# Kernel optimization log

Hardware: AMD Instinct MI355X
Metric: run time of the kernel (lower is better)

## Reference

```python
import jax, jax.numpy as jnp
import numpy as np

B, C, H, W = 16, 256, 56, 56
PH, PW = 7, 7            # partition (window) size
HEADS, DH = 8, 32        # n_heads = C // head_dim
P = PH * PW              # tokens per window = 49
GH, GW = H // PH, W // PW
G = GH * GW              # number of windows = 64
MLP = 4                  # mlp_ratio
EPS = 1e-5
SCALE = C ** (-0.5)      # note: torch code scales by feat_dim, not head_dim


def _rel_index(h, w):
    coords = np.stack(np.meshgrid(np.arange(h), np.arange(w), indexing='ij'))  # [2,h,w]
    cf = coords.reshape(2, -1)
    rel = cf[:, :, None] - cf[:, None, :]              # [2,P,P]
    rel = rel.transpose(1, 2, 0)
    rel[:, :, 0] += h - 1
    rel[:, :, 1] += w - 1
    rel[:, :, 0] *= 2 * w - 1
    return rel.sum(-1).astype(np.int32)                # [P,P]


def setup_inputs() -> dict:
    key = jax.random.key(0)
    ks = jax.random.split(key, 8)
    std = 0.02
    return {
        'x': jax.random.normal(ks[0], (B, C, H, W), jnp.float32),
        'ln1_g': jnp.ones((C,), jnp.float32),
        'ln1_b': jnp.zeros((C,), jnp.float32),
        'wqkv': jax.random.normal(ks[1], (C, 3 * C), jnp.float32) * std,
        'bqkv': jnp.zeros((3 * C,), jnp.float32),
        'wmerge': jax.random.normal(ks[2], (C, C), jnp.float32) * std,
        'bmerge': jnp.zeros((C,), jnp.float32),
        'bias_table': jax.random.normal(ks[3], ((2 * PH - 1) * (2 * PW - 1), HEADS), jnp.float32) * std,
        'ln2_g': jnp.ones((C,), jnp.float32),
        'ln2_b': jnp.zeros((C,), jnp.float32),
        'w1': jax.random.normal(ks[4], (C, MLP * C), jnp.float32) * std,
        'b1': jnp.zeros((MLP * C,), jnp.float32),
        'w2': jax.random.normal(ks[5], (MLP * C, C), jnp.float32) * std,
        'b2': jnp.zeros((C,), jnp.float32),
        'rel_idx': jnp.asarray(_rel_index(PH, PW)),
    }


def _layernorm(x, g, b):
    mu = jnp.mean(x, axis=-1, keepdims=True)
    var = jnp.var(x, axis=-1, keepdims=True)
    return (x - mu) * jax.lax.rsqrt(var + EPS) * g + b


def reference(x, ln1_g, ln1_b, wqkv, bqkv, wmerge, bmerge, bias_table,
              ln2_g, ln2_b, w1, b1, w2, b2, rel_idx):
    # --- window partition: [B,C,H,W] -> [B,G,P,C]
    xw = x.reshape(B, C, GH, PH, GW, PW).transpose(0, 2, 4, 3, 5, 1).reshape(B, G, P, C)

    # --- relative-position attention block
    y = _layernorm(xw, ln1_g, ln1_b)
    qkv = y @ wqkv + bqkv                               # [B,G,P,3C]
    q, k, v = jnp.split(qkv, 3, axis=-1)
    q = q.reshape(B, G, P, HEADS, DH)
    k = k.reshape(B, G, P, HEADS, DH) * SCALE
    v = v.reshape(B, G, P, HEADS, DH)
    scores = jnp.einsum('bgihd,bgjhd->bghij', q, k)     # [B,G,H,P,P]
    bias = bias_table[rel_idx].transpose(2, 0, 1)       # [H,P,P]
    attn = jax.nn.softmax(scores + bias[None, None], axis=-1)
    out = jnp.einsum('bghij,bgjhd->bgihd', attn, v).reshape(B, G, P, C)
    out = out @ wmerge + bmerge
    xw = xw + out

    # --- MLP block
    z = _layernorm(xw, ln2_g, ln2_b)
    z = jax.nn.gelu(z @ w1 + b1, approximate=False) @ w2 + b2
    xw = xw + z

    # --- window departition: [B,G,P,C] -> [B,C,H,W]
    xo = xw.reshape(B, GH, GW, PH, PW, C).transpose(0, 5, 1, 3, 2, 4).reshape(B, C, H, W)
    return xo
```

## Files before the change

kernel.cpp:

```cpp
#include <hip/hip_runtime.h>
#include <hip/hip_bf16.h>

#define B_      16
#define C_      256
#define H_      56
#define W_      56
#define HW_     3136
#define G_      64
#define P_      49
#define NTOK    50176
#define HEADS_  8
#define DH_     32
#define SCALE_  0.0625f
#define EPS_    1e-5f

typedef short bf16x8 __attribute__((ext_vector_type(8)));
typedef short bf16x4_t __attribute__((ext_vector_type(4)));
typedef float f32x4  __attribute__((ext_vector_type(4)));
using bf16 = __hip_bfloat16;

__device__ __forceinline__ void gload16(const void* g, void* l) {
  __builtin_amdgcn_global_load_lds((const __attribute__((address_space(1))) void*)g,
                                   (__attribute__((address_space(3))) void*)l, 16, 0, 0);
}
__device__ __forceinline__ float b2f(short s) {
  union { float f; unsigned u; } v; v.u = ((unsigned)(unsigned short)s) << 16; return v.f;
}
__device__ __forceinline__ short f2b(float f) {
  union { float f; unsigned u; } v; v.f = f;
  unsigned r = (v.u + 0x7FFFu + ((v.u >> 16) & 1u)) >> 16;
  return (short)r;
}

__global__ __launch_bounds__(256)
void prep_kernel(const float* __restrict__ wqkv, const float* __restrict__ wmerge,
                 const float* __restrict__ w1, const float* __restrict__ w2,
                 const float* __restrict__ btab, const int* __restrict__ relidx,
                 bf16* __restrict__ wqkvT, bf16* __restrict__ wmergeT,
                 bf16* __restrict__ w1T, bf16* __restrict__ w2T,
                 short* __restrict__ bt)
{
  int idx = blockIdx.x * 256 + threadIdx.x;
  if (idx < 196608) { int n = idx >> 8, k = idx & 255;
    wqkvT[idx] = __float2bfloat16(wqkv[k * 768 + n]); return; }
  idx -= 196608;
  if (idx < 65536) { int n = idx >> 8, k = idx & 255;
    wmergeT[idx] = __float2bfloat16(wmerge[k * 256 + n]); return; }
  idx -= 65536;
  if (idx < 262144) { int n = idx >> 8, k = idx & 255;
    w1T[idx] = __float2bfloat16(w1[k * 1024 + n]); return; }
  idx -= 262144;
  if (idx < 262144) { int n = idx >> 10, k = idx & 1023;
    w2T[idx] = __float2bfloat16(w2[k * 256 + n]); return; }
  idx -= 262144;
  if (idx < 32768) {
    int h = idx >> 12, rest = idx & 4095;
    int key = rest >> 6, col = rest & 63;
    int q = col >> 2, qni = col & 3;
    int query = qni * 16 + q;
    float v = 0.f;
    if (key < P_ && query < P_) v = btab[relidx[query * P_ + key] * HEADS_ + h];
    bt[idx] = f2b(v);
  }
}

__global__ __launch_bounds__(256)
void ingest_kernel(const float* __restrict__ x, const float* __restrict__ gam,
                   const float* __restrict__ bet, short* __restrict__ xtok,
                   short* __restrict__ y)
{
  __shared__ short Lt[56 * 260];
  const int h = blockIdx.x % 56, b = blockIdx.x / 56;
  const int tid = threadIdx.x;

  const float* xb = x + (size_t)b * 256 * HW_ + h * 56;
#pragma unroll
  for (int i = 0; i < 14; i++) {
    int idx = i * 256 + tid;
    int c = idx / 14, w4 = idx - c * 14;
    float4 v = *(const float4*)(xb + (size_t)c * HW_ + w4 * 4);
    Lt[(w4 * 4 + 0) * 260 + c] = f2b(v.x);
    Lt[(w4 * 4 + 1) * 260 + c] = f2b(v.y);
    Lt[(w4 * 4 + 2) * 260 + c] = f2b(v.z);
    Lt[(w4 * 4 + 3) * 260 + c] = f2b(v.w);
  }
  __syncthreads();

  const int lane = tid & 63, wv = tid >> 6;
  float4 gv = *(const float4*)(gam + lane * 4);
  float4 bv = *(const float4*)(bet + lane * 4);
  const int hdiv = h / 7, hmod = h - hdiv * 7;

  for (int t = 0; t < 14; t++) {
    int w = wv * 14 + t;
    bf16x4_t raw = *(const bf16x4_t*)&Lt[w * 260 + lane * 4];
    float f0 = b2f(raw[0]), f1 = b2f(raw[1]), f2 = b2f(raw[2]), f3 = b2f(raw[3]);
    float sum = f0 + f1 + f2 + f3;
    float sq  = f0*f0 + f1*f1 + f2*f2 + f3*f3;
#pragma unroll
    for (int off = 32; off > 0; off >>= 1) {
      sum += __shfl_xor(sum, off, 64);
      sq  += __shfl_xor(sq,  off, 64);
    }
    float mu = sum * (1.0f / 256.0f);
    float var = sq * (1.0f / 256.0f) - mu * mu;
    float rs = rsqrtf(var + EPS_);
    int wdiv = w / 7, wmod = w - wdiv * 7;
    int tok = b * HW_ + (hdiv * 8 + wdiv) * P_ + hmod * 7 + wmod;
    *(bf16x4_t*)(xtok + (size_t)tok * 256 + lane * 4) = raw;
    bf16x4_t o;
    o[0] = f2b((f0 - mu) * rs * gv.x + bv.x);
    o[1] = f2b((f1 - mu) * rs * gv.y + bv.y);
    o[2] = f2b((f2 - mu) * rs * gv.z + bv.z);
    o[3] = f2b((f3 - mu) * rs * gv.w + bv.w);
    *(bf16x4_t*)(y + (size_t)tok * 256 + lane * 4) = o;
  }
}

__global__ __launch_bounds__(256)
void ln2_kernel(const short* __restrict__ xw, const float* __restrict__ gam,
                const float* __restrict__ bet, short* __restrict__ z)
{
  const int t = blockIdx.x * 4 + (threadIdx.x >> 6);
  const int lane = threadIdx.x & 63;
  bf16x4_t raw = *(const bf16x4_t*)(xw + (size_t)t * 256 + lane * 4);
  float v[4];
#pragma unroll
  for (int j = 0; j < 4; j++) v[j] = b2f(raw[j]);
  float sum = v[0] + v[1] + v[2] + v[3];
  float sq  = v[0]*v[0] + v[1]*v[1] + v[2]*v[2] + v[3]*v[3];
#pragma unroll
  for (int off = 32; off > 0; off >>= 1) {
    sum += __shfl_xor(sum, off, 64);
    sq  += __shfl_xor(sq,  off, 64);
  }
  float mu = sum * (1.0f / 256.0f);
  float var = sq * (1.0f / 256.0f) - mu * mu;
  float rs = rsqrtf(var + EPS_);
  bf16x4_t o;
#pragma unroll
  for (int j = 0; j < 4; j++) {
    int c = lane * 4 + j;
    o[j] = f2b((v[j] - mu) * rs * gam[c] + bet[c]);
  }
  *(bf16x4_t*)(z + (size_t)t * 256 + lane * 4) = o;
}

__global__ __launch_bounds__(256)
void egress_kernel(const short* __restrict__ outtok, float* __restrict__ out)
{
  const int h = blockIdx.x % 56, b = blockIdx.x / 56;
  const int w = threadIdx.x & 63, cblk = threadIdx.x >> 6;
  const bool act = w < 56;
  const int wcl = act ? w : 55;
  const int tok = b * HW_ + ((h / 7) * 8 + wcl / 7) * P_ + (h % 7) * 7 + (wcl % 7);
  const short* src = outtok + (size_t)tok * 256 + cblk * 64;
  float* dst = out + ((size_t)b * 256 + cblk * 64) * HW_ + h * 56 + w;
#pragma unroll
  for (int j0 = 0; j0 < 64; j0 += 8) {
    bf16x8 r = *(const bf16x8*)(src + j0);
#pragma unroll
    for (int jj = 0; jj < 8; jj++)
      if (act) dst[(size_t)(j0 + jj) * HW_] = b2f(r[jj]);
  }
}

__global__ __launch_bounds__(64)
void attn_kernel(const short* __restrict__ qkv, const short* __restrict__ bt,
                 short* __restrict__ out)
{
  __shared__ short Pbuf[64 * 72];
  const int bid = blockIdx.x;
  const int h = bid & 7;
  const int t0 = (bid >> 3) * P_;
  const int lane = threadIdx.x;
  const int g = lane >> 4, q = lane & 15;

  const short* qb = qkv + (size_t)t0 * 768 + h * 32;

  bf16x8 vf[2][2];
#pragma unroll
  for (int kkt = 0; kkt < 2; kkt++)
#pragma unroll
    for (int n2 = 0; n2 < 2; n2++)
#pragma unroll
      for (int jj = 0; jj < 8; jj++) {
        int key = kkt * 32 + 8 * g + jj; key = key > 48 ? 48 : key;
        vf[kkt][n2][jj] = qb[(size_t)key * 768 + 512 + n2 * 16 + q];
      }

  bf16x8 kf[4], qf[4];
#pragma unroll
  for (int mi = 0; mi < 4; mi++) {
    int r_ = mi * 16 + q; r_ = r_ > 48 ? 48 : r_;
    kf[mi] = *(const bf16x8*)(qb + (size_t)r_ * 768 + 256 + 8 * g);
  }
#pragma unroll
  for (int ni = 0; ni < 4; ni++) {
    int r_ = ni * 16 + q; r_ = r_ > 48 ? 48 : r_;
    qf[ni] = *(const bf16x8*)(qb + (size_t)r_ * 768 + 8 * g);
  }

  f32x4 sacc[4][4] = {};
#pragma unroll
  for (int mi = 0; mi < 4; mi++)
#pragma unroll
    for (int ni = 0; ni < 4; ni++)
      sacc[mi][ni] = __builtin_amdgcn_mfma_f32_16x16x32_bf16(kf[mi], qf[ni], sacc[mi][ni], 0, 0, 0);

  float mx[4] = {-1e30f, -1e30f, -1e30f, -1e30f};
  const short* btb = bt + (size_t)(h * 64) * 64 + q * 4;
#pragma unroll
  for (int mi = 0; mi < 4; mi++)
#pragma unroll
    for (int r = 0; r < 4; r++) {
      int key = mi * 16 + 4 * g + r;
      bf16x4_t bv = *(const bf16x4_t*)(btb + key * 64);
      bool valid = key < P_;
#pragma unroll
      for (int ni = 0; ni < 4; ni++) {
        float s = valid ? fmaf(sacc[mi][ni][r], SCALE_, b2f(bv[ni])) : -1e30f;
        sacc[mi][ni][r] = s;
        mx[ni] = fmaxf(mx[ni], s);
      }
    }
#pragma unroll
  for (int ni = 0; ni < 4; ni++) {
    mx[ni] = fmaxf(mx[ni], __shfl_xor(mx[ni], 16, 64));
    mx[ni] = fmaxf(mx[ni], __shfl_xor(mx[ni], 32, 64));
  }
  float sm[4] = {0.f, 0.f, 0.f, 0.f};
#pragma unroll
  for (int mi = 0; mi < 4; mi++)
#pragma unroll
    for (int ni = 0; ni < 4; ni++)
#pragma unroll
      for (int r = 0; r < 4; r++) {
        float p = __expf(sacc[mi][ni][r] - mx[ni]);
        sacc[mi][ni][r] = p;
        sm[ni] += p;
      }
#pragma unroll
  for (int ni = 0; ni < 4; ni++) {
    sm[ni] += __shfl_xor(sm[ni], 16, 64);
    sm[ni] += __shfl_xor(sm[ni], 32, 64);
    sm[ni] = 1.0f / sm[ni];
  }
#pragma unroll
  for (int ni = 0; ni < 4; ni++)
#pragma unroll
    for (int mi = 0; mi < 4; mi++) {
      bf16x4_t pv;
#pragma unroll
      for (int r = 0; r < 4; r++) pv[r] = f2b(sacc[mi][ni][r] * sm[ni]);
      *(bf16x4_t*)&Pbuf[(ni * 16 + q) * 72 + mi * 16 + 4 * g] = pv;
    }
  __syncthreads();

  f32x4 oacc[4][2] = {};
#pragma unroll
  for (int kkt = 0; kkt < 2; kkt++) {
    bf16x8 paf[4];
#pragma unroll
    for (int qi = 0; qi < 4; qi++)
      paf[qi] = *(const bf16x8*)&Pbuf[(qi * 16 + q) * 72 + kkt * 32 + 8 * g];
#pragma unroll
    for (int qi = 0; qi < 4; qi++)
#pragma unroll
      for (int n2 = 0; n2 < 2; n2++)
        oacc[qi][n2] = __builtin_amdgcn_mfma_f32_16x16x32_bf16(paf[qi], vf[kkt][n2], oacc[qi][n2], 0, 0, 0);
  }

  short* ob = out + (size_t)t0 * 256 + h * 32;
#pragma unroll
  for (int qi = 0; qi < 4; qi++)
#pragma unroll
    for (int r = 0; r < 4; r++) {
      int query = qi * 16 + 4 * g + r;
      if (query < P_) {
#pragma unroll
        for (int n2 = 0; n2 < 2; n2++)
          ob[(size_t)query * 256 + n2 * 16 + q] = f2b(oacc[qi][n2][r]);
      }
    }
}

template<int EPI, int WN>
__global__ __launch_bounds__(128 * WN)
void gemm_kernel(const bf16* __restrict__ A, const bf16* __restrict__ Wt,
                 const float* __restrict__ bias, int N, int K,
                 bf16* __restrict__ outb, short* __restrict__ res_io)
{
  constexpr int THREADS = 128 * WN;
  constexpr int BN = 64 * WN;
  constexpr int RPP = THREADS / 4;
  constexpr int APASS = 128 / RPP;
  __shared__ __align__(16) bf16 As[2][128 * 32];
  __shared__ __align__(16) bf16 Bs[2][BN * 32];
  const int tid = threadIdx.x;
  const int lane = tid & 63;
  const int wave = tid >> 6;
  const int wr = wave / WN, wc = wave % WN;
  const int bm = blockIdx.y * 128, bn = blockIdx.x * BN;

  f32x4 acc[4][4] = {};

  const int trow = tid >> 2;
  const int tcol = ((tid & 3) ^ ((tid >> 3) & 3)) * 8;
  const bf16* aA[APASS];
#pragma unroll
  for (int p = 0; p < APASS; p++)
    aA[p] = A + (size_t)(bm + p * RPP + trow) * K + tcol;
  const bf16* aB0 = Wt + (size_t)(bn + trow) * K + tcol;
  const bf16* aB1 = Wt + (size_t)(bn + RPP + trow) * K + tcol;
  const int dOff = tid * 8;

  const int kc_sw = ((lane >> 4) ^ ((lane >> 1) & 3)) * 8;
  const int rA = wr * 64 + (lane & 15);
  const int rB = wc * 64 + (lane & 15);

  const int nt = K >> 5;

#pragma unroll
  for (int p = 0; p < APASS; p++) gload16(aA[p], &As[0][p * RPP * 32 + dOff]);
  gload16(aB0, &Bs[0][dOff]);
  gload16(aB1, &Bs[0][RPP * 32 + dOff]);
  __syncthreads();

  for (int t = 0; t < nt; ++t) {
    const int cur = t & 1;
    if (t + 1 < nt) {
      const int k1 = (t + 1) << 5;
      const int nxt = cur ^ 1;
#pragma unroll
      for (int p = 0; p < APASS; p++) gload16(aA[p] + k1, &As[nxt][p * RPP * 32 + dOff]);
      gload16(aB0 + k1, &Bs[nxt][dOff]);
      gload16(aB1 + k1, &Bs[nxt][RPP * 32 + dOff]);
    }
    bf16x8 af[4], bfr[4];
#pragma unroll
    for (int i = 0; i < 4; i++) {
      af[i]  = *(const bf16x8*)(&As[cur][(rA + i * 16) * 32 + kc_sw]);
      bfr[i] = *(const bf16x8*)(&Bs[cur][(rB + i * 16) * 32 + kc_sw]);
    }
#pragma unroll
    for (int mi = 0; mi < 4; mi++)
#pragma unroll
      for (int ni = 0; ni < 4; ni++)
        acc[mi][ni] = __builtin_amdgcn_mfma_f32_16x16x32_bf16(af[mi], bfr[ni], acc[mi][ni], 0, 0, 0);
    __syncthreads();
  }

#pragma unroll
  for (int mi = 0; mi < 4; mi++) {
#pragma unroll
    for (int ni = 0; ni < 4; ni++) {
#pragma unroll
      for (int r = 0; r < 4; r++) {
        const int row = bm + wr * 64 + mi * 16 + (lane >> 4) * 4 + r;
        const int col = bn + wc * 64 + ni * 16 + (lane & 15);
        float v = acc[mi][ni][r] + bias[col];
        if (EPI == 0) {
          outb[(size_t)row * N + col] = __float2bfloat16(v);
        } else if (EPI == 1) {
          float gv = 0.5f * v * (1.0f + erff(v * 0.70710678118f));
          outb[(size_t)row * N + col] = __float2bfloat16(gv);
        } else {
          size_t o = (size_t)row * 256 + col;
          res_io[o] = f2b(v + b2f(res_io[o]));
        }
      }
    }
  }
}

extern "C" void kernel_launch(void* const* d_in, const int* in_sizes, int n_in,
                              void* d_out, int out_size, void* d_ws, size_t ws_size,
                              hipStream_t stream)
{
  const float* x      = (const float*)d_in[0];
  const float* ln1_g  = (const float*)d_in[1];
  const float* ln1_b  = (const float*)d_in[2];
  const float* wqkv   = (const float*)d_in[3];
  const float* bqkv   = (const float*)d_in[4];
  const float* wmerge = (const float*)d_in[5];
  const float* bmerge = (const float*)d_in[6];
  const float* btab   = (const float*)d_in[7];
  const float* ln2_g  = (const float*)d_in[8];
  const float* ln2_b  = (const float*)d_in[9];
  const float* w1     = (const float*)d_in[10];
  const float* b1     = (const float*)d_in[11];
  const float* w2     = (const float*)d_in[12];
  const float* b2     = (const float*)d_in[13];
  const int*   relidx = (const int*)d_in[14];
  float* out = (float*)d_out;

  char* ws = (char*)d_ws;
  bf16*  wqkvT   = (bf16*)(ws);
  bf16*  wmergeT = (bf16*)(ws + 393216);
  bf16*  w1T     = (bf16*)(ws + 524288);
  bf16*  w2T     = (bf16*)(ws + 1048576);
  short* battn   = (short*)(ws + 1572864);
  short* R1      = (short*)(ws + 1638400);
  short* R2      = (short*)(ws + 27328512);
  short* qkvc    = (short*)(ws + 53018624);
  short* attnc   = (short*)(ws + 91553792);
  short* hbuf    = (short*)(ws + 53018624);

  prep_kernel<<<3200, 256, 0, stream>>>(wqkv, wmerge, w1, w2, btab, relidx,
                                        wqkvT, wmergeT, w1T, w2T, battn);

  ingest_kernel<<<896, 256, 0, stream>>>(x, ln1_g, ln1_b, R1, R2);

  for (int c = 0; c < 2; ++c) {
    size_t r0 = (size_t)c * 25088;
    gemm_kernel<0, 4><<<dim3(3, 196), 512, 0, stream>>>(
        (const bf16*)(R2 + r0 * 256), wqkvT, bqkv, 768, 256, (bf16*)qkvc, nullptr);
    attn_kernel<<<4096, 64, 0, stream>>>(qkvc, battn, attnc);
    gemm_kernel<2, 2><<<dim3(2, 196), 256, 0, stream>>>(
        (const bf16*)attnc, wmergeT, bmerge, 256, 256, nullptr, R1 + r0 * 256);
  }

  ln2_kernel<<<NTOK / 4, 256, 0, stream>>>(R1, ln2_g, ln2_b, R2);

  for (int c = 0; c < 2; ++c) {
    size_t r0 = (size_t)c * 25088;
    gemm_kernel<1, 4><<<dim3(4, 196), 512, 0, stream>>>(
        (const bf16*)(R2 + r0 * 256), w1T, b1, 1024, 256, (bf16*)hbuf, nullptr);
    gemm_kernel<2, 2><<<dim3(2, 196), 256, 0, stream>>>(
        (const bf16*)hbuf, w2T, b2, 256, 1024, nullptr, R1 + r0 * 256);
  }

  egress_kernel<<<896, 256, 0, stream>>>(R1, out);
}
```

Measured before the change: 285.6 us.

## Use 128x128 tiles with 64-deep K steps in all GEMMs

Result: slower. 310.7 us (+8.8%).

```diff
diff --git a/kernel.cpp b/kernel.cpp
--- a/kernel.cpp
+++ b/kernel.cpp
@@ -285,69 +285,73 @@
     }
 }
 
-template<int EPI, int WN>
-__global__ __launch_bounds__(128 * WN)
-void gemm_kernel(const bf16* __restrict__ A, const bf16* __restrict__ Wt,
-                 const float* __restrict__ bias, int N, int K,
-                 bf16* __restrict__ outb, short* __restrict__ res_io)
-{
-  constexpr int THREADS = 128 * WN;
-  constexpr int BN = 64 * WN;
-  constexpr int RPP = THREADS / 4;
-  constexpr int APASS = 128 / RPP;
-  __shared__ __align__(16) bf16 As[2][128 * 32];
-  __shared__ __align__(16) bf16 Bs[2][BN * 32];
+template<int EPI>
+__global__ __launch_bounds__(256)
+void gemm64_kernel(const bf16* __restrict__ A, const bf16* __restrict__ Wt,
+                   const float* __restrict__ bias, int N, int K,
+                   bf16* __restrict__ outb, short* __restrict__ res_io)
+{
+  __shared__ __align__(16) bf16 As[2][128 * 64];
+  __shared__ __align__(16) bf16 Bs[2][128 * 64];
   const int tid = threadIdx.x;
   const int lane = tid & 63;
   const int wave = tid >> 6;
-  const int wr = wave / WN, wc = wave % WN;
-  const int bm = blockIdx.y * 128, bn = blockIdx.x * BN;
+  const int wr = wave >> 1, wc = wave & 1;
+  const int l15 = lane & 15, g = lane >> 4;
+  const int bm = blockIdx.y * 128, bn = blockIdx.x * 128;
 
   f32x4 acc[4][4] = {};
 
-  const int trow = tid >> 2;
-  const int tcol = ((tid & 3) ^ ((tid >> 3) & 3)) * 8;
-  const bf16* aA[APASS];
-#pragma unroll
-  for (int p = 0; p < APASS; p++)
-    aA[p] = A + (size_t)(bm + p * RPP + trow) * K + tcol;
-  const bf16* aB0 = Wt + (size_t)(bn + trow) * K + tcol;
-  const bf16* aB1 = Wt + (size_t)(bn + RPP + trow) * K + tcol;
-  const int dOff = tid * 8;
-
-  const int kc_sw = ((lane >> 4) ^ ((lane >> 1) & 3)) * 8;
-  const int rA = wr * 64 + (lane & 15);
-  const int rB = wc * 64 + (lane & 15);
-
-  const int nt = K >> 5;
-
-#pragma unroll
-  for (int p = 0; p < APASS; p++) gload16(aA[p], &As[0][p * RPP * 32 + dOff]);
-  gload16(aB0, &Bs[0][dOff]);
-  gload16(aB1, &Bs[0][RPP * 32 + dOff]);
+  const bf16* aA[4];
+  const bf16* aB[4];
+#pragma unroll
+  for (int p = 0; p < 4; p++) {
+    int idx = p * 256 + tid;
+    int row = idx >> 3, cs = idx & 7;
+    int scol = (cs ^ (row & 7)) * 8;
+    aA[p] = A  + (size_t)(bm + row) * K + scol;
+    aB[p] = Wt + (size_t)(bn + row) * K + scol;
+  }
+
+  const int nt = K >> 6;
+
+#pragma unroll
+  for (int p = 0; p < 4; p++) {
+    gload16(aA[p], &As[0][(p * 256 + tid) * 8]);
+    gload16(aB[p], &Bs[0][(p * 256 + tid) * 8]);
+  }
   __syncthreads();
+
+  const int rA = wr * 64 + l15;
+  const int rB = wc * 64 + l15;
+  const int x7 = l15 & 7;
 
   for (int t = 0; t < nt; ++t) {
     const int cur = t & 1;
     if (t + 1 < nt) {
-      const int k1 = (t + 1) << 5;
+      const int k1 = (t + 1) << 6;
       const int nxt = cur ^ 1;
 #pragma unroll
-      for (int p = 0; p < APASS; p++) gload16(aA[p] + k1, &As[nxt][p * RPP * 32 + dOff]);
-      gload16(aB0 + k1, &Bs[nxt][dOff]);
-      gload16(aB1 + k1, &Bs[nxt][RPP * 32 + dOff]);
-    }
-    bf16x8 af[4], bfr[4];
-#pragma unroll
-    for (int i = 0; i < 4; i++) {
-      af[i]  = *(const bf16x8*)(&As[cur][(rA + i * 16) * 32 + kc_sw]);
-      bfr[i] = *(const bf16x8*)(&Bs[cur][(rB + i * 16) * 32 + kc_sw]);
-    }
-#pragma unroll
-    for (int mi = 0; mi < 4; mi++)
-#pragma unroll
-      for (int ni = 0; ni < 4; ni++)
-        acc[mi][ni] = __builtin_amdgcn_mfma_f32_16x16x32_bf16(af[mi], bfr[ni], acc[mi][ni], 0, 0, 0);
+      for (int p = 0; p < 4; p++) {
+        gload16(aA[p] + k1, &As[nxt][(p * 256 + tid) * 8]);
+        gload16(aB[p] + k1, &Bs[nxt][(p * 256 + tid) * 8]);
+      }
+    }
+#pragma unroll
+    for (int s = 0; s < 2; ++s) {
+      const int sl = ((s * 4 + g) ^ x7) * 8;
+      bf16x8 af[4], bfr[4];
+#pragma unroll
+      for (int i = 0; i < 4; i++) {
+        af[i]  = *(const bf16x8*)(&As[cur][(rA + i * 16) * 64 + sl]);
+        bfr[i] = *(const bf16x8*)(&Bs[cur][(rB + i * 16) * 64 + sl]);
+      }
+#pragma unroll
+      for (int mi = 0; mi < 4; mi++)
+#pragma unroll
+        for (int ni = 0; ni < 4; ni++)
+          acc[mi][ni] = __builtin_amdgcn_mfma_f32_16x16x32_bf16(af[mi], bfr[ni], acc[mi][ni], 0, 0, 0);
+    }
     __syncthreads();
   }
 
@@ -357,8 +361,8 @@
     for (int ni = 0; ni < 4; ni++) {
 #pragma unroll
       for (int r = 0; r < 4; r++) {
-        const int row = bm + wr * 64 + mi * 16 + (lane >> 4) * 4 + r;
-        const int col = bn + wc * 64 + ni * 16 + (lane & 15);
+        const int row = bm + wr * 64 + mi * 16 + g * 4 + r;
+        const int col = bn + wc * 64 + ni * 16 + l15;
         float v = acc[mi][ni][r] + bias[col];
         if (EPI == 0) {
           outb[(size_t)row * N + col] = __float2bfloat16(v);
@@ -414,10 +418,10 @@
 
   for (int c = 0; c < 2; ++c) {
     size_t r0 = (size_t)c * 25088;
-    gemm_kernel<0, 4><<<dim3(3, 196), 512, 0, stream>>>(
+    gemm64_kernel<0><<<dim3(6, 196), 256, 0, stream>>>(
         (const bf16*)(R2 + r0 * 256), wqkvT, bqkv, 768, 256, (bf16*)qkvc, nullptr);
     attn_kernel<<<4096, 64, 0, stream>>>(qkvc, battn, attnc);
-    gemm_kernel<2, 2><<<dim3(2, 196), 256, 0, stream>>>(
+    gemm64_kernel<2><<<dim3(2, 196), 256, 0, stream>>>(
         (const bf16*)attnc, wmergeT, bmerge, 256, 256, nullptr, R1 + r0 * 256);
   }
 
@@ -425,9 +429,9 @@
 
   for (int c = 0; c < 2; ++c) {
     size_t r0 = (size_t)c * 25088;
-    gemm_kernel<1, 4><<<dim3(4, 196), 512, 0, stream>>>(
+    gemm64_kernel<1><<<dim3(8, 196), 256, 0, stream>>>(
         (const bf16*)(R2 + r0 * 256), w1T, b1, 1024, 256, (bf16*)hbuf, nullptr);
-    gemm_kernel<2, 2><<<dim3(2, 196), 256, 0, stream>>>(
+    gemm64_kernel<2><<<dim3(2, 196), 256, 0, stream>>>(
         (const bf16*)hbuf, w2T, b2, 256, 1024, nullptr, R1 + r0 * 256);
   }
 
```

## Prefetch two K-tiles ahead in GEMM with explicit vmcnt waits

Applied to the files above, without the earlier changes.

Measured after the change: 284.4 us. No clear change (-0.4%).

```diff
diff --git a/kernel.cpp b/kernel.cpp
--- a/kernel.cpp
+++ b/kernel.cpp
@@ -295,8 +295,11 @@
   constexpr int BN = 64 * WN;
   constexpr int RPP = THREADS / 4;
   constexpr int APASS = 128 / RPP;
+  constexpr int BPASS = BN / RPP;
+  constexpr int NLOADS = APASS + BPASS;
   __shared__ __align__(16) bf16 As[2][128 * 32];
   __shared__ __align__(16) bf16 Bs[2][BN * 32];
+
   const int tid = threadIdx.x;
   const int lane = tid & 63;
   const int wave = tid >> 6;
@@ -311,32 +314,38 @@
 #pragma unroll
   for (int p = 0; p < APASS; p++)
     aA[p] = A + (size_t)(bm + p * RPP + trow) * K + tcol;
-  const bf16* aB0 = Wt + (size_t)(bn + trow) * K + tcol;
-  const bf16* aB1 = Wt + (size_t)(bn + RPP + trow) * K + tcol;
+  const bf16* aB[BPASS];
+#pragma unroll
+  for (int p = 0; p < BPASS; p++)
+    aB[p] = Wt + (size_t)(bn + p * RPP + trow) * K + tcol;
   const int dOff = tid * 8;
 
   const int kc_sw = ((lane >> 4) ^ ((lane >> 1) & 3)) * 8;
-  const int rA = wr * 64 + (lane & 15);
-  const int rB = wc * 64 + (lane & 15);
+  const int l15 = lane & 15, g = lane >> 4;
+  const int rA = wr * 64 + l15;
+  const int rB = wc * 64 + l15;
 
   const int nt = K >> 5;
 
 #pragma unroll
   for (int p = 0; p < APASS; p++) gload16(aA[p], &As[0][p * RPP * 32 + dOff]);
-  gload16(aB0, &Bs[0][dOff]);
-  gload16(aB1, &Bs[0][RPP * 32 + dOff]);
-  __syncthreads();
+#pragma unroll
+  for (int p = 0; p < BPASS; p++) gload16(aB[p], &Bs[0][p * RPP * 32 + dOff]);
+#pragma unroll
+  for (int p = 0; p < APASS; p++) gload16(aA[p] + 32, &As[1][p * RPP * 32 + dOff]);
+#pragma unroll
+  for (int p = 0; p < BPASS; p++) gload16(aB[p] + 32, &Bs[1][p * RPP * 32 + dOff]);
 
   for (int t = 0; t < nt; ++t) {
     const int cur = t & 1;
     if (t + 1 < nt) {
-      const int k1 = (t + 1) << 5;
-      const int nxt = cur ^ 1;
-#pragma unroll
-      for (int p = 0; p < APASS; p++) gload16(aA[p] + k1, &As[nxt][p * RPP * 32 + dOff]);
-      gload16(aB0 + k1, &Bs[nxt][dOff]);
-      gload16(aB1 + k1, &Bs[nxt][RPP * 32 + dOff]);
-    }
+      if constexpr (NLOADS == 3) asm volatile("s_waitcnt vmcnt(3)" ::: "memory");
+      else                       asm volatile("s_waitcnt vmcnt(4)" ::: "memory");
+    } else {
+      asm volatile("s_waitcnt vmcnt(0)" ::: "memory");
+    }
+    __builtin_amdgcn_s_barrier();
+
     bf16x8 af[4], bfr[4];
 #pragma unroll
     for (int i = 0; i < 4; i++) {
@@ -348,7 +357,15 @@
 #pragma unroll
       for (int ni = 0; ni < 4; ni++)
         acc[mi][ni] = __builtin_amdgcn_mfma_f32_16x16x32_bf16(af[mi], bfr[ni], acc[mi][ni], 0, 0, 0);
-    __syncthreads();
+
+    __builtin_amdgcn_s_barrier();
+    if (t + 2 < nt) {
+      const int k2 = (t + 2) << 5;
+#pragma unroll
+      for (int p = 0; p < APASS; p++) gload16(aA[p] + k2, &As[cur][p * RPP * 32 + dOff]);
+#pragma unroll
+      for (int p = 0; p < BPASS; p++) gload16(aB[p] + k2, &Bs[cur][p * RPP * 32 + dOff]);
+    }
   }
 
 #pragma unroll
@@ -357,8 +374,8 @@
     for (int ni = 0; ni < 4; ni++) {
 #pragma unroll
       for (int r = 0; r < 4; r++) {
-        const int row = bm + wr * 64 + mi * 16 + (lane >> 4) * 4 + r;
-        const int col = bn + wc * 64 + ni * 16 + (lane & 15);
+        const int row = bm + wr * 64 + mi * 16 + g * 4 + r;
+        const int col = bn + wc * 64 + ni * 16 + l15;
         float v = acc[mi][ni][r] + bias[col];
         if (EPI == 0) {
           outb[(size_t)row * N + col] = __float2bfloat16(v);
```
